# Kernel tuning notes

Measured on AMD Instinct MI355X. Metric: run time of the kernel, lower is better.

Reference implementation:

```python
import jax, jax.numpy as jnp
import numpy as np

B, S, D, H, ATT = 2048, 200, 64, 64, 64  # batch, hist_len, embed_dim, hidden, attention_size


def _xavier(k, shape):
    fan_out, fan_in = shape
    std = (2.0 / (fan_in + fan_out)) ** 0.5
    return (jax.random.normal(k, shape, jnp.float32) * std).astype(jnp.float32)


def setup_inputs() -> dict:
    key = jax.random.key(0)
    ks = jax.random.split(key, 12)
    return {
        "behavior": jax.random.normal(ks[0], (B, S, D), jnp.float32),
        "target": jax.random.normal(ks[1], (B, D), jnp.float32),
        "lengths": jax.random.randint(ks[2], (B,), 1, S + 1),
        # Interest-extraction GRU (torch nn.GRU layout: gates [r|z|n])
        "Wih": _xavier(ks[3], (3 * H, D)),
        "Whh": _xavier(ks[4], (3 * H, H)),
        "bih": jnp.zeros((3 * H,), jnp.float32),
        "bhh": jnp.zeros((3 * H,), jnp.float32),
        # Evolution attention MLP: Linear(H+D -> ATT) + ReLU + Linear(ATT -> 1, no bias)
        "A1": _xavier(ks[5], (ATT, H + D)),
        "b1": jnp.zeros((ATT,), jnp.float32),
        "A2": _xavier(ks[6], (1, ATT)),
        # Attentional GRU gates: Linear(input+hidden -> hidden)
        "Wr": _xavier(ks[7], (H, 2 * H)),
        "br": jnp.zeros((H,), jnp.float32),
        "Wz": _xavier(ks[8], (H, 2 * H)),
        "bz": jnp.zeros((H,), jnp.float32),
        "Wn": _xavier(ks[9], (H, 2 * H)),
        "bn": jnp.zeros((H,), jnp.float32),
    }


def _forward(behavior, target, lengths, Wih, Whh, bih, bhh, A1, b1, A2, Wr, br, Wz, bz, Wn, bn):
    Bsz, Slen, Din = behavior.shape
    Hs = Whh.shape[1]
    dt = behavior.dtype
    # (B, S) validity mask for padded positions (pack_padded_sequence semantics)
    mask = jnp.arange(Slen)[None, :] < lengths[:, None]

    # ---- Interest Extraction: masked GRU over time (lax.scan) ----
    gi_all = jnp.einsum('bsd,gd->sbg', behavior, Wih) + bih  # (S, B, 3H), input gates precomputed
    valid_t = jnp.moveaxis(mask, 0, 1)[..., None]            # (S, B, 1)

    def gru_step(h, inp):
        gi, v = inp
        gh = h @ Whh.T + bhh
        ir, iz, inn = jnp.split(gi, 3, axis=-1)
        hr, hz, hn = jnp.split(gh, 3, axis=-1)
        r = jax.nn.sigmoid(ir + hr)
        z = jax.nn.sigmoid(iz + hz)
        n = jnp.tanh(inn + r * hn)
        hnew = (1.0 - z) * n + z * h
        hnew = jnp.where(v, hnew, h)          # hold state past sequence end
        out = jnp.where(v, hnew, jnp.zeros_like(hnew))  # padded outputs are zero
        return hnew, out

    h0 = jnp.zeros((Bsz, Hs), dt)
    _, outs = jax.lax.scan(gru_step, h0, (gi_all, valid_t))  # outs: (S, B, H)
    hidden_states = jnp.moveaxis(outs, 0, 1)                 # (B, S, H)

    # ---- Interest Evolution: concat-MLP attention + masked softmax ----
    tgt = jnp.broadcast_to(target[:, None, :], (Bsz, Slen, Din))
    comb = jnp.concatenate([hidden_states, tgt], axis=-1)    # (B, S, H+D)
    att = jax.nn.relu(comb @ A1.T + b1) @ A2.T               # (B, S, 1)
    scores = jnp.where(mask, att[..., 0], jnp.asarray(-1e9, dt))
    att_w = jax.nn.softmax(scores, axis=1)[..., None]        # (B, S, 1)

    # ---- Attentional GRU scan over timesteps ----
    w_t = jnp.moveaxis(att_w, 0, 1)                          # (S, B, 1)

    def agru_step(h, inp):
        hi, ai = inp                                         # (B,H), (B,1)
        cat = jnp.concatenate([hi, h], axis=-1)
        r = jax.nn.sigmoid(cat @ Wr.T + br)
        z = jax.nn.sigmoid(cat @ Wz.T + bz) * ai             # attention-gated update gate
        catr = jnp.concatenate([hi, r * h], axis=-1)
        n = jnp.tanh(catr @ Wn.T + bn)
        return (1.0 - z) * h + z * n, None

    h_final, _ = jax.lax.scan(agru_step, jnp.zeros((Bsz, Hs), dt), (outs, w_t))
    return h_final  # (B, H)


def reference(behavior, target, lengths, Wih, Whh, bih, bhh, A1, b1, A2, Wr, br, Wz, bz, Wn, bn):
    return _forward(behavior, target, lengths, Wih, Whh, bih, bhh, A1, b1, A2, Wr, br, Wz, bz, Wn, bn)
```

## Files before the change

### kernel.cpp

```cpp
#include <hip/hip_runtime.h>

#define SLEN 200
#define NB   2048
#define CS   40

typedef short  bf8s   __attribute__((ext_vector_type(8)));
typedef __bf16 bf16x8 __attribute__((ext_vector_type(8)));
typedef float  f4     __attribute__((ext_vector_type(4)));

__device__ __forceinline__ short fb1(float x){ __bf16 b=(__bf16)x; return __builtin_bit_cast(short,b); }
__device__ __forceinline__ float b2f(unsigned short b){
  return __builtin_bit_cast(float, ((unsigned int)b)<<16);
}
__device__ __forceinline__ float ldf(const void* p, long i, bool bf){
  return bf ? b2f(((const unsigned short*)p)[i]) : ((const float*)p)[i];
}
__device__ __forceinline__ bf8s loadfrag(const void* p, long i, bool bf){
  bf8s r;
  if (bf) {
    r = *(const bf8s*)((const unsigned short*)p + i);
  } else {
    const float* q = (const float*)p + i;
#pragma unroll
    for (int k=0;k<8;k++) r[k] = fb1(q[k]);
  }
  return r;
}
__device__ __forceinline__ float rcp_(float x){ return __builtin_amdgcn_rcpf(x); }
__device__ __forceinline__ float sigm(float x){ return rcp_(1.f + __expf(-x)); }
__device__ __forceinline__ float tanh_(float x){ return 1.f - 2.f*rcp_(1.f + __expf(2.f*x)); }
__device__ __forceinline__ f4 MF(bf8s a, bf8s b, f4 c){
  return __builtin_amdgcn_mfma_f32_16x16x32_bf16(
    __builtin_bit_cast(bf16x8,a), __builtin_bit_cast(bf16x8,b), c, 0,0,0);
}
__device__ __forceinline__ void sync_lds(){
  asm volatile("s_waitcnt lgkmcnt(0)" ::: "memory");
  __builtin_amdgcn_s_barrier();
  __builtin_amdgcn_sched_barrier(0);
}

__global__ __launch_bounds__(256)
void k0_prep(const unsigned int* wds, int nw, const int* lengths, int* flag, int* perm){
  __shared__ int hist[256];
  __shared__ int base[256];
  __shared__ int cnt[256];
  __shared__ int wsum[4];
  const int tid = threadIdx.x;
  int c = 0;
  for (int i=tid;i<nw;i+=256){
    unsigned e = (wds[i] >> 7) & 0xFFu;
    c += (e >= 96u && e <= 160u) ? 1 : 0;
  }
  cnt[tid]=c; hist[tid]=0;
  __syncthreads();
  for (int s=128;s>0;s>>=1){
    if (tid<s) cnt[tid]+=cnt[tid+s];
    __syncthreads();
  }
  if (tid==0) flag[0] = (cnt[0]*2 > nw) ? 1 : 0;
  for (int i=tid;i<NB;i+=256) atomicAdd(&hist[lengths[i]&255],1);
  __syncthreads();
  {
    const int lane=tid&63, w=tid>>6;
    int v = hist[tid];
    int sum = v;
#pragma unroll
    for (int d=1; d<64; d<<=1){
      int o = __shfl_up(sum, d);
      if (lane >= d) sum += o;
    }
    if (lane==63) wsum[w]=sum;
    __syncthreads();
    int woff=0;
#pragma unroll
    for (int k=0;k<4;++k) if (k<w) woff+=wsum[k];
    base[tid] = woff + sum - v;
  }
  __syncthreads();
  for (int i=tid;i<NB;i+=256){
    int l=lengths[i]&255;
    int p=atomicAdd(&base[l],1);
    perm[p]=i;
  }
}

__global__ __launch_bounds__(256,1)
void fused(const void* behavior, const void* target, const int* lengths,
           const void* Wih, const void* Whh, const void* bih, const void* bhh,
           const void* A1, const void* b1, const void* A2,
           const void* Wr, const void* br, const void* Wz, const void* bz,
           const void* Wn, const void* bn,
           const int* perm, const int* flag,
           unsigned short* hidden, float* out){
  const bool bf = flag[0]!=0;
  const int tid=threadIdx.x, lane=tid&63, w=tid>>6, l15=lane&15, q=lane>>4;
  const int g0 = blockIdx.x*8;
  const int xrow = ((l15>>2)<<1)|(l15&1);

  __shared__ alignas(16) unsigned short x_s[2][CS][8][72];
  __shared__ alignas(16) unsigned short h_lds[2][16][72];
  __shared__ alignas(16) unsigned short h_hist[16][8][72];
  __shared__ alignas(16) unsigned short rh_lds[16][72];
  __shared__ float att_l[8][200];
  __shared__ float score_s[8][208];
  __shared__ float ct_s[8][64];
  __shared__ alignas(16) unsigned short tg_s[8][72];
  __shared__ float a2_s[64];
  __shared__ int rows8[8], lens8[8];

  if (tid<8){ int r=perm[g0+tid]; rows8[tid]=r; lens8[tid]=lengths[r]; }
  for (int i=tid;i<2*16*72;i+=256) ((unsigned short*)h_lds)[i]=0;
  for (int i=tid;i<16*72;i+=256)   ((unsigned short*)rh_lds)[i]=0;
  __syncthreads();

  int maxlen=1;
#pragma unroll
  for (int i=0;i<8;++i) maxlen = max(maxlen, lens8[i]);
  const int ml1 = maxlen-1;
  const int jc = w*16 + l15;

  const unsigned short* bp=(const unsigned short*)behavior;
  const float*          fp=(const float*)behavior;

  uint4 xr[10];
  auto issue_g = [&](const unsigned short* src, int t0){
#pragma unroll
    for (int it=0; it<10; ++it){
      int i=it*256+tid, row=i/320, k=i-row*320;
      int t=min(t0+(k>>3), ml1), d0=(k&7)*8;
      xr[it] = *(const uint4*)(src + (long)rows8[row]*(SLEN*64) + t*64 + d0);
    }
  };
  auto write_s = [&](int b_){
#pragma unroll
    for (int it=0; it<10; ++it){
      int i=it*256+tid, row=i/320, k=i-row*320;
      *(uint4*)&x_s[b_][k>>3][row][(k&7)*8] = xr[it];
    }
  };
  auto f32_stage = [&](int b_, int t0){
#pragma unroll
    for (int it=0; it<10; ++it){
      int i=it*256+tid, row=i/320, k=i-row*320;
      int t=min(t0+(k>>3), ml1), d0=(k&7)*8;
      const float* s = fp + (long)rows8[row]*(SLEN*64) + t*64 + d0;
      f4 a=*(const f4*)s, b2=*(const f4*)(s+4);
      bf8s v;
#pragma unroll
      for (int j=0;j<4;++j){ v[j]=fb1(a[j]); v[4+j]=fb1(b2[j]); }
      *(bf8s*)&x_s[b_][k>>3][row][d0] = v;
    }
  };
  auto dump_window = [&](int tbase){
    int dt = tid>>5, row=(tid>>2)&7, cs=(tid&3)*16;
    int t = tbase+dt;
    if (t < lens8[row]){
      uint4 v0 = *(const uint4*)&h_hist[t&15][row][cs];
      uint4 v1 = *(const uint4*)&h_hist[t&15][row][cs+8];
      long o = ((long)rows8[row]*SLEN + t)*64 + cs;
      *(uint4*)&hidden[o]   = v0;
      *(uint4*)&hidden[o+8] = v1;
    }
  };

  {
    bf8s wif[3][2], whf[3][2];
#pragma unroll
    for (int G=0;G<3;++G)
#pragma unroll
      for (int kf=0;kf<2;++kf){
        long off = (long)(G*64+jc)*64 + kf*32 + q*8;
        wif[G][kf] = loadfrag(Wih, off, bf);
        whf[G][kf] = loadfrag(Whh, off, bf);
      }
    const float Br  = ldf(bih,jc,bf)+ldf(bhh,jc,bf);
    const float Bz  = ldf(bih,64+jc,bf)+ldf(bhh,64+jc,bf);
    const float Bin = ldf(bih,128+jc,bf);
    const float Bhn = ldf(bhh,128+jc,bf);
    int Ln2[2];
#pragma unroll
    for (int i=0;i<2;++i) Ln2[i] = lens8[2*q+i];
    float hreg[2]={0.f,0.f};

    if (bf){ issue_g(bp,0); write_s(0); if (maxlen>CS) issue_g(bp,CS); }
    else   { f32_stage(0,0); }
    __syncthreads();

    int c=0;
    for (int t0=0; t0<maxlen; t0+=CS, ++c){
      const int tend = min(t0+CS, maxlen);
      for (int t=t0; t<tend; ++t){
        if ((t&7)==0 && t>=8) dump_window(t-8);
        const int tc = t-t0;
        bf8s xa0 = *(const bf8s*)&x_s[c&1][tc][xrow][q*8];
        bf8s xa1 = *(const bf8s*)&x_s[c&1][tc][xrow][32+q*8];
        bf8s ha0 = *(const bf8s*)&h_lds[t&1][l15][q*8];
        bf8s ha1 = *(const bf8s*)&h_lds[t&1][l15][32+q*8];

        f4 Tr  = {Br,Br,Br,Br};
        f4 Tz  = {Bz,Bz,Bz,Bz};
        f4 Txn = {Bin,Bin,Bin,Bin};
        f4 Thn = {Bhn,Bhn,Bhn,Bhn};
        Tr =MF(xa0,wif[0][0],Tr );  Tr =MF(xa1,wif[0][1],Tr );
        Tz =MF(xa0,wif[1][0],Tz );  Tz =MF(xa1,wif[1][1],Tz );
        Txn=MF(xa0,wif[2][0],Txn);  Txn=MF(xa1,wif[2][1],Txn);
        Tr =MF(ha0,whf[0][0],Tr );  Tr =MF(ha1,whf[0][1],Tr );
        Tz =MF(ha0,whf[1][0],Tz );  Tz =MF(ha1,whf[1][1],Tz );
        Thn=MF(ha0,whf[2][0],Thn); Thn=MF(ha1,whf[2][1],Thn);

        const int nb_=(t+1)&1;
#pragma unroll
        for (int i=0;i<2;++i){
          const int ar = 4*q+i;
          const int b_ = 2*q+i;
          float rg = sigm(Tr[i]);
          float zg = sigm(Tz[i]);
          float ng = tanh_(Txn[i] + rg*Thn[i]);
          float hold = hreg[i];
          float hnew = (1.f-zg)*ng + zg*hold;
          float hv = (t < Ln2[i]) ? hnew : hold;
          hreg[i] = hv;
          unsigned short hb16 = (unsigned short)fb1(hv);
          h_lds[nb_][ar][jc] = hb16;
          h_hist[t&15][b_][jc] = hb16;
        }
        sync_lds();
      }
      if (t0+CS < maxlen){
        if (bf){ write_s((c+1)&1); if (t0+2*CS < maxlen) issue_g(bp, t0+2*CS); }
        else   { f32_stage((c+1)&1, t0+CS); }
        sync_lds();
      }
    }
    dump_window((maxlen-1)&~7);
    asm volatile("s_waitcnt vmcnt(0)" ::: "memory");
  }
  __syncthreads();

  for (int i=tid;i<8*64;i+=256){
    int r=i>>6, c2=i&63;
    tg_s[r][c2] = (unsigned short)fb1(ldf(target,(long)rows8[r]*64 + c2, bf));
  }
  if (tid<64) a2_s[tid]=ldf(A2,tid,bf);
  __syncthreads();

  {
    {
      bf8s a1c0 = loadfrag(A1,(long)(w*16+l15)*128 + 64 + q*8, bf);
      bf8s a1c1 = loadfrag(A1,(long)(w*16+l15)*128 + 96 + q*8, bf);
      bf8s tgf0 = *(const bf8s*)&tg_s[l15&7][q*8];
      bf8s tgf1 = *(const bf8s*)&tg_s[l15&7][32+q*8];
      f4 Dct={0.f,0.f,0.f,0.f};
      Dct=MF(a1c0,tgf0,Dct);
      Dct=MF(a1c1,tgf1,Dct);
      if (l15<8){
#pragma unroll
        for (int i=0;i<4;++i)
          ct_s[l15][w*16+4*q+i] = Dct[i] + ldf(b1,w*16+4*q+i,bf);
      }
    }
    bf8s a1f[4][2];
#pragma unroll
    for (int nt=0;nt<4;++nt)
#pragma unroll
      for (int kf=0;kf<2;++kf)
        a1f[nt][kf] = loadfrag(A1,(long)(nt*16+l15)*128 + kf*32 + q*8, bf);
    __syncthreads();

#pragma unroll
    for (int rr=0;rr<2;++rr){
      int r = 2*w+rr, lenr = lens8[r];
      int mtr = (lenr+15)>>4; if (mtr>13) mtr=13;
      for (int mt=0; mt<mtr; ++mt){
        const unsigned short* hp = &hidden[((long)rows8[r]*SLEN + mt*16+l15)*64 + q*8];
        bf8s h0 = *(const bf8s*)hp;
        bf8s h1 = *(const bf8s*)(hp+32);
        f4 acc[4];
#pragma unroll
        for (int nt=0;nt<4;++nt){
          f4 a={0.f,0.f,0.f,0.f};
          a=MF(h0,a1f[nt][0],a); a=MF(h1,a1f[nt][1],a); acc[nt]=a;
        }
#pragma unroll
        for (int i=0;i<4;++i){
          float s=0.f;
#pragma unroll
          for (int nt=0;nt<4;++nt){
            int au = nt*16 + l15;
            s += fmaxf(acc[nt][i]+ct_s[r][au],0.f)*a2_s[au];
          }
#pragma unroll
          for (int d=1; d<16; d<<=1) s += __shfl_xor(s,d);
          if (l15==0) score_s[r][mt*16+4*q+i] = s;
        }
      }
      int t0=lane, t1=64+lane, t2=128+lane, t3=192+lane;
      float v0=(t0<lenr)?score_s[r][t0]:-3e38f;
      float v1=(t1<lenr)?score_s[r][t1]:-3e38f;
      float v2=(t2<lenr)?score_s[r][t2]:-3e38f;
      float v3=(t3<lenr)?score_s[r][t3]:-3e38f;
      float m = fmaxf(fmaxf(v0,v1),fmaxf(v2,v3));
#pragma unroll
      for (int d=32;d>0;d>>=1) m = fmaxf(m,__shfl_xor(m,d));
      float e0=(t0<lenr)?__expf(v0-m):0.f;
      float e1=(t1<lenr)?__expf(v1-m):0.f;
      float e2=(t2<lenr)?__expf(v2-m):0.f;
      float e3=(t3<lenr)?__expf(v3-m):0.f;
      float S = e0+e1+e2+e3;
#pragma unroll
      for (int d=32;d>0;d>>=1) S += __shfl_xor(S,d);
      float Si = rcp_(S);
      att_l[r][t0] = e0*Si;
      att_l[r][t1] = e1*Si;
      if (t2<200) att_l[r][t2] = e2*Si;
      if (t3<200) att_l[r][t3] = e3*Si;
    }
  }
  __syncthreads();

  for (int i=tid;i<2*16*72;i+=256) ((unsigned short*)h_lds)[i]=0;

  bf8s wrf[2][2], wzf[2][2], wnf[2][2];
#pragma unroll
  for (int hh=0;hh<2;++hh)
#pragma unroll
    for (int kf=0;kf<2;++kf){
      long off = (long)jc*128 + hh*64 + kf*32 + q*8;
      wrf[hh][kf]=loadfrag(Wr,off,bf);
      wzf[hh][kf]=loadfrag(Wz,off,bf);
      wnf[hh][kf]=loadfrag(Wn,off,bf);
    }
  const float Brv=ldf(br,jc,bf), Bzv=ldf(bz,jc,bf), Bnv=ldf(bn,jc,bf);

  float h3[2]={0.f,0.f};
  const long hbase = (long)rows8[xrow]*(SLEN*64) + q*8;
  bf8s hb00,hb01,hb10,hb11;
  {
    long o1 = hbase + (long)min(1,ml1)*64;
    hb00=*(const bf8s*)(hidden+hbase); hb01=*(const bf8s*)(hidden+hbase+32);
    hb10=*(const bf8s*)(hidden+o1);    hb11=*(const bf8s*)(hidden+o1+32);
  }
  __syncthreads();

  for (int t=0;t<maxlen;++t){
    long po = hbase + (long)min(t+2,ml1)*64;
    bf8s pN0 = *(const bf8s*)(hidden+po);
    bf8s pN1 = *(const bf8s*)(hidden+po+32);

    bf8s ha0=*(const bf8s*)&h_lds[t&1][l15][q*8];
    bf8s ha1=*(const bf8s*)&h_lds[t&1][l15][32+q*8];

    f4 Tr = {Brv,Brv,Brv,Brv};
    f4 Tz = {Bzv,Bzv,Bzv,Bzv};
    f4 Tn = {Bnv,Bnv,Bnv,Bnv};
    Tr=MF(hb00,wrf[0][0],Tr); Tr=MF(hb01,wrf[0][1],Tr);
    Tz=MF(hb00,wzf[0][0],Tz); Tz=MF(hb01,wzf[0][1],Tz);
    Tn=MF(hb00,wnf[0][0],Tn); Tn=MF(hb01,wnf[0][1],Tn);
    Tr=MF(ha0, wrf[1][0],Tr); Tr=MF(ha1, wrf[1][1],Tr);
    Tz=MF(ha0, wzf[1][0],Tz); Tz=MF(ha1, wzf[1][1],Tz);

    float zs[2], hs[2];
#pragma unroll
    for (int i=0;i<2;++i){
      const int ar = 4*q+i;
      const int b_ = 2*q+i;
      float rg = sigm(Tr[i]);
      float ai = att_l[b_][t];
      float zg = sigm(Tz[i]) * ai;
      float hold = h3[i];
      zs[i]=zg; hs[i]=hold;
      rh_lds[ar][jc] = (unsigned short)fb1(rg*hold);
    }
    sync_lds();

    bf8s ra0 = *(const bf8s*)&rh_lds[l15][q*8];
    bf8s ra1 = *(const bf8s*)&rh_lds[l15][32+q*8];
    Tn=MF(ra0,wnf[1][0],Tn); Tn=MF(ra1,wnf[1][1],Tn);

    const int nb_=(t+1)&1;
#pragma unroll
    for (int i=0;i<2;++i){
      const int ar = 4*q+i;
      float ng = tanh_(Tn[i]);
      float hnew = (zs[i]==0.f) ? hs[i] : hs[i] + zs[i]*(ng - hs[i]);
      h3[i] = hnew;
      h_lds[nb_][ar][jc] = (unsigned short)fb1(hnew);
    }
    hb00=hb10; hb01=hb11; hb10=pN0; hb11=pN1;
    sync_lds();
  }
#pragma unroll
  for (int i=0;i<2;++i)
    out[(long)rows8[2*q+i]*64 + jc] = h3[i];
}

extern "C" void kernel_launch(void* const* d_in, const int* in_sizes, int n_in,
                              void* d_out, int out_size, void* d_ws, size_t ws_size,
                              hipStream_t stream) {
  const void* behavior = d_in[0];
  const void* target   = d_in[1];
  const int*  lengths  = (const int*)d_in[2];
  const void* Wih = d_in[3];
  const void* Whh = d_in[4];
  const void* bih = d_in[5];
  const void* bhh = d_in[6];
  const void* A1  = d_in[7];
  const void* b1  = d_in[8];
  const void* A2  = d_in[9];
  const void* Wr  = d_in[10];
  const void* br  = d_in[11];
  const void* Wz  = d_in[12];
  const void* bz  = d_in[13];
  const void* Wn  = d_in[14];
  const void* bn  = d_in[15];

  int* flag = (int*)d_ws;
  unsigned short* hidden = (unsigned short*)((char*)d_ws + 256);
  int* perm = (int*)((char*)d_ws + 256 + (size_t)NB*SLEN*64*2);
  size_t needed = 256 + (size_t)NB*SLEN*64*2 + (size_t)NB*4;
  if (ws_size < needed) return;

  k0_prep<<<1, 256, 0, stream>>>((const unsigned int*)behavior, 4096, lengths, flag, perm);
  fused<<<NB/8, 256, 0, stream>>>(behavior, target, lengths,
                                  Wih, Whh, bih, bhh, A1, b1, A2,
                                  Wr, br, Wz, bz, Wn, bn,
                                  perm, flag, hidden, (float*)d_out);
}
```

Baseline: 226.4 us.

## Split each block to four sequences, raise occupancy, prefetch x from global directly

Each block now handles 4 batch rows instead of 8, and the grid becomes 512 blocks. Launch bounds are raised to allow 3 blocks per CU, and the chunked LDS staging of behavior is removed. Input rows are instead prefetched two steps ahead straight into registers. The aim is more concurrent recurrent chains per CU, to hide the serial per-timestep latency, and a smaller LDS footprint. In exchange, MFMA tiles are only a quarter used (one useful row per 16-row group), and per-step global loads sit on the recurrence path.

New measurement: 347.9 us. +53.7%, slower.

```diff
diff --git a/kernel.cpp b/kernel.cpp
--- a/kernel.cpp
+++ b/kernel.cpp
@@ -2,7 +2,6 @@
 
 #define SLEN 200
 #define NB   2048
-#define CS   40
 
 typedef short  bf8s   __attribute__((ext_vector_type(8)));
 typedef __bf16 bf16x8 __attribute__((ext_vector_type(8)));
@@ -84,7 +83,7 @@
   }
 }
 
-__global__ __launch_bounds__(256,1)
+__global__ __launch_bounds__(256,3)
 void fused(const void* behavior, const void* target, const int* lengths,
            const void* Wih, const void* Whh, const void* bih, const void* bhh,
            const void* A1, const void* b1, const void* A2,
@@ -94,72 +93,40 @@
            unsigned short* hidden, float* out){
   const bool bf = flag[0]!=0;
   const int tid=threadIdx.x, lane=tid&63, w=tid>>6, l15=lane&15, q=lane>>4;
-  const int g0 = blockIdx.x*8;
-  const int xrow = ((l15>>2)<<1)|(l15&1);
-
-  __shared__ alignas(16) unsigned short x_s[2][CS][8][72];
+  const int g0 = (blockIdx.x & 255)*8 + (blockIdx.x >> 8)*4;
+  const int xb = l15>>2;
+
   __shared__ alignas(16) unsigned short h_lds[2][16][72];
-  __shared__ alignas(16) unsigned short h_hist[16][8][72];
+  __shared__ alignas(16) unsigned short h_hist[16][4][72];
   __shared__ alignas(16) unsigned short rh_lds[16][72];
-  __shared__ float att_l[8][200];
-  __shared__ float score_s[8][208];
-  __shared__ float ct_s[8][64];
-  __shared__ alignas(16) unsigned short tg_s[8][72];
+  __shared__ float att_l[4][200];
+  __shared__ float score_s[4][208];
+  __shared__ float ct_s[4][64];
+  __shared__ alignas(16) unsigned short tg_s[4][72];
   __shared__ float a2_s[64];
-  __shared__ int rows8[8], lens8[8];
-
-  if (tid<8){ int r=perm[g0+tid]; rows8[tid]=r; lens8[tid]=lengths[r]; }
+  __shared__ int rows4[4], lens4[4];
+
+  if (tid<4){ int r=perm[g0+tid]; rows4[tid]=r; lens4[tid]=lengths[r]; }
   for (int i=tid;i<2*16*72;i+=256) ((unsigned short*)h_lds)[i]=0;
   for (int i=tid;i<16*72;i+=256)   ((unsigned short*)rh_lds)[i]=0;
   __syncthreads();
 
   int maxlen=1;
 #pragma unroll
-  for (int i=0;i<8;++i) maxlen = max(maxlen, lens8[i]);
+  for (int i=0;i<4;++i) maxlen = max(maxlen, lens4[i]);
   const int ml1 = maxlen-1;
   const int jc = w*16 + l15;
 
   const unsigned short* bp=(const unsigned short*)behavior;
   const float*          fp=(const float*)behavior;
 
-  uint4 xr[10];
-  auto issue_g = [&](const unsigned short* src, int t0){
-#pragma unroll
-    for (int it=0; it<10; ++it){
-      int i=it*256+tid, row=i/320, k=i-row*320;
-      int t=min(t0+(k>>3), ml1), d0=(k&7)*8;
-      xr[it] = *(const uint4*)(src + (long)rows8[row]*(SLEN*64) + t*64 + d0);
-    }
-  };
-  auto write_s = [&](int b_){
-#pragma unroll
-    for (int it=0; it<10; ++it){
-      int i=it*256+tid, row=i/320, k=i-row*320;
-      *(uint4*)&x_s[b_][k>>3][row][(k&7)*8] = xr[it];
-    }
-  };
-  auto f32_stage = [&](int b_, int t0){
-#pragma unroll
-    for (int it=0; it<10; ++it){
-      int i=it*256+tid, row=i/320, k=i-row*320;
-      int t=min(t0+(k>>3), ml1), d0=(k&7)*8;
-      const float* s = fp + (long)rows8[row]*(SLEN*64) + t*64 + d0;
-      f4 a=*(const f4*)s, b2=*(const f4*)(s+4);
-      bf8s v;
-#pragma unroll
-      for (int j=0;j<4;++j){ v[j]=fb1(a[j]); v[4+j]=fb1(b2[j]); }
-      *(bf8s*)&x_s[b_][k>>3][row][d0] = v;
-    }
-  };
   auto dump_window = [&](int tbase){
-    int dt = tid>>5, row=(tid>>2)&7, cs=(tid&3)*16;
+    int dt = tid>>5, row=(tid>>3)&3, cs=(tid&7)*8;
     int t = tbase+dt;
-    if (t < lens8[row]){
+    if (t < lens4[row]){
       uint4 v0 = *(const uint4*)&h_hist[t&15][row][cs];
-      uint4 v1 = *(const uint4*)&h_hist[t&15][row][cs+8];
-      long o = ((long)rows8[row]*SLEN + t)*64 + cs;
-      *(uint4*)&hidden[o]   = v0;
-      *(uint4*)&hidden[o+8] = v1;
+      long o = ((long)rows4[row]*SLEN + t)*64 + cs;
+      *(uint4*)&hidden[o] = v0;
     }
   };
 
@@ -177,69 +144,77 @@
     const float Bz  = ldf(bih,64+jc,bf)+ldf(bhh,64+jc,bf);
     const float Bin = ldf(bih,128+jc,bf);
     const float Bhn = ldf(bhh,128+jc,bf);
-    int Ln2[2];
-#pragma unroll
-    for (int i=0;i<2;++i) Ln2[i] = lens8[2*q+i];
-    float hreg[2]={0.f,0.f};
-
-    if (bf){ issue_g(bp,0); write_s(0); if (maxlen>CS) issue_g(bp,CS); }
-    else   { f32_stage(0,0); }
-    __syncthreads();
-
-    int c=0;
-    for (int t0=0; t0<maxlen; t0+=CS, ++c){
-      const int tend = min(t0+CS, maxlen);
-      for (int t=t0; t<tend; ++t){
-        if ((t&7)==0 && t>=8) dump_window(t-8);
-        const int tc = t-t0;
-        bf8s xa0 = *(const bf8s*)&x_s[c&1][tc][xrow][q*8];
-        bf8s xa1 = *(const bf8s*)&x_s[c&1][tc][xrow][32+q*8];
-        bf8s ha0 = *(const bf8s*)&h_lds[t&1][l15][q*8];
-        bf8s ha1 = *(const bf8s*)&h_lds[t&1][l15][32+q*8];
-
-        f4 Tr  = {Br,Br,Br,Br};
-        f4 Tz  = {Bz,Bz,Bz,Bz};
-        f4 Txn = {Bin,Bin,Bin,Bin};
-        f4 Thn = {Bhn,Bhn,Bhn,Bhn};
-        Tr =MF(xa0,wif[0][0],Tr );  Tr =MF(xa1,wif[0][1],Tr );
-        Tz =MF(xa0,wif[1][0],Tz );  Tz =MF(xa1,wif[1][1],Tz );
-        Txn=MF(xa0,wif[2][0],Txn);  Txn=MF(xa1,wif[2][1],Txn);
-        Tr =MF(ha0,whf[0][0],Tr );  Tr =MF(ha1,whf[0][1],Tr );
-        Tz =MF(ha0,whf[1][0],Tz );  Tz =MF(ha1,whf[1][1],Tz );
-        Thn=MF(ha0,whf[2][0],Thn); Thn=MF(ha1,whf[2][1],Thn);
-
-        const int nb_=(t+1)&1;
-#pragma unroll
-        for (int i=0;i<2;++i){
-          const int ar = 4*q+i;
-          const int b_ = 2*q+i;
-          float rg = sigm(Tr[i]);
-          float zg = sigm(Tz[i]);
-          float ng = tanh_(Txn[i] + rg*Thn[i]);
-          float hold = hreg[i];
-          float hnew = (1.f-zg)*ng + zg*hold;
-          float hv = (t < Ln2[i]) ? hnew : hold;
-          hreg[i] = hv;
-          unsigned short hb16 = (unsigned short)fb1(hv);
-          h_lds[nb_][ar][jc] = hb16;
-          h_hist[t&15][b_][jc] = hb16;
+    const int LnQ = lens4[q];
+    float hreg = 0.f;
+
+    const long xbase = (long)rows4[xb]*(SLEN*64) + q*8;
+    bf8s xC0,xC1,xN0,xN1;
+    f4 c0,c1,c2,c3, n0,n1,n2,n3;
+    {
+      long o0=xbase, o1=xbase+(long)min(1,ml1)*64;
+      if (bf){
+        xC0=*(const bf8s*)(bp+o0); xC1=*(const bf8s*)(bp+o0+32);
+        xN0=*(const bf8s*)(bp+o1); xN1=*(const bf8s*)(bp+o1+32);
+      } else {
+        c0=*(const f4*)(fp+o0); c1=*(const f4*)(fp+o0+4); c2=*(const f4*)(fp+o0+32); c3=*(const f4*)(fp+o0+36);
+        n0=*(const f4*)(fp+o1); n1=*(const f4*)(fp+o1+4); n2=*(const f4*)(fp+o1+32); n3=*(const f4*)(fp+o1+36);
+      }
+    }
+
+    for (int t=0;t<maxlen;++t){
+      if ((t&7)==0 && t>=8) dump_window(t-8);
+      long po = xbase + (long)min(t+2,ml1)*64;
+      bf8s pN0,pN1; f4 p0,p1,p2,p3;
+      if (bf){ pN0=*(const bf8s*)(bp+po); pN1=*(const bf8s*)(bp+po+32); }
+      else   { p0=*(const f4*)(fp+po); p1=*(const f4*)(fp+po+4); p2=*(const f4*)(fp+po+32); p3=*(const f4*)(fp+po+36); }
+
+      bf8s ha0 = *(const bf8s*)&h_lds[t&1][l15][q*8];
+      bf8s ha1 = *(const bf8s*)&h_lds[t&1][l15][32+q*8];
+      bf8s xa0, xa1;
+      if (bf){ xa0=xC0; xa1=xC1; }
+      else {
+#pragma unroll
+        for (int j=0;j<4;++j){
+          xa0[j]=fb1(c0[j]); xa0[4+j]=fb1(c1[j]);
+          xa1[j]=fb1(c2[j]); xa1[4+j]=fb1(c3[j]);
         }
-        sync_lds();
-      }
-      if (t0+CS < maxlen){
-        if (bf){ write_s((c+1)&1); if (t0+2*CS < maxlen) issue_g(bp, t0+2*CS); }
-        else   { f32_stage((c+1)&1, t0+CS); }
-        sync_lds();
-      }
+      }
+
+      f4 Tr  = {Br,Br,Br,Br};
+      f4 Tz  = {Bz,Bz,Bz,Bz};
+      f4 Txn = {Bin,Bin,Bin,Bin};
+      f4 Thn = {Bhn,Bhn,Bhn,Bhn};
+      Tr =MF(xa0,wif[0][0],Tr );  Tr =MF(xa1,wif[0][1],Tr );
+      Tz =MF(xa0,wif[1][0],Tz );  Tz =MF(xa1,wif[1][1],Tz );
+      Txn=MF(xa0,wif[2][0],Txn);  Txn=MF(xa1,wif[2][1],Txn);
+      Tr =MF(ha0,whf[0][0],Tr );  Tr =MF(ha1,whf[0][1],Tr );
+      Tz =MF(ha0,whf[1][0],Tz );  Tz =MF(ha1,whf[1][1],Tz );
+      Thn=MF(ha0,whf[2][0],Thn);  Thn=MF(ha1,whf[2][1],Thn);
+
+      const int nb_=(t+1)&1;
+      {
+        float rg = sigm(Tr[0]);
+        float zg = sigm(Tz[0]);
+        float ng = tanh_(Txn[0] + rg*Thn[0]);
+        float hnew = (1.f-zg)*ng + zg*hreg;
+        float hv = (t < LnQ) ? hnew : hreg;
+        hreg = hv;
+        unsigned short hb16 = (unsigned short)fb1(hv);
+        h_lds[nb_][4*q][jc] = hb16;
+        h_hist[t&15][q][jc] = hb16;
+      }
+      if (bf){ xC0=xN0; xC1=xN1; xN0=pN0; xN1=pN1; }
+      else   { c0=n0;c1=n1;c2=n2;c3=n3; n0=p0;n1=p1;n2=p2;n3=p3; }
+      sync_lds();
     }
     dump_window((maxlen-1)&~7);
     asm volatile("s_waitcnt vmcnt(0)" ::: "memory");
   }
   __syncthreads();
 
-  for (int i=tid;i<8*64;i+=256){
+  for (int i=tid;i<4*64;i+=256){
     int r=i>>6, c2=i&63;
-    tg_s[r][c2] = (unsigned short)fb1(ldf(target,(long)rows8[r]*64 + c2, bf));
+    tg_s[r][c2] = (unsigned short)fb1(ldf(target,(long)rows4[r]*64 + c2, bf));
   }
   if (tid<64) a2_s[tid]=ldf(A2,tid,bf);
   __syncthreads();
@@ -248,12 +223,12 @@
     {
       bf8s a1c0 = loadfrag(A1,(long)(w*16+l15)*128 + 64 + q*8, bf);
       bf8s a1c1 = loadfrag(A1,(long)(w*16+l15)*128 + 96 + q*8, bf);
-      bf8s tgf0 = *(const bf8s*)&tg_s[l15&7][q*8];
-      bf8s tgf1 = *(const bf8s*)&tg_s[l15&7][32+q*8];
+      bf8s tgf0 = *(const bf8s*)&tg_s[l15&3][q*8];
+      bf8s tgf1 = *(const bf8s*)&tg_s[l15&3][32+q*8];
       f4 Dct={0.f,0.f,0.f,0.f};
       Dct=MF(a1c0,tgf0,Dct);
       Dct=MF(a1c1,tgf1,Dct);
-      if (l15<8){
+      if (l15<4){
 #pragma unroll
         for (int i=0;i<4;++i)
           ct_s[l15][w*16+4*q+i] = Dct[i] + ldf(b1,w*16+4*q+i,bf);
@@ -267,54 +242,51 @@
         a1f[nt][kf] = loadfrag(A1,(long)(nt*16+l15)*128 + kf*32 + q*8, bf);
     __syncthreads();
 
-#pragma unroll
-    for (int rr=0;rr<2;++rr){
-      int r = 2*w+rr, lenr = lens8[r];
-      int mtr = (lenr+15)>>4; if (mtr>13) mtr=13;
-      for (int mt=0; mt<mtr; ++mt){
-        const unsigned short* hp = &hidden[((long)rows8[r]*SLEN + mt*16+l15)*64 + q*8];
-        bf8s h0 = *(const bf8s*)hp;
-        bf8s h1 = *(const bf8s*)(hp+32);
-        f4 acc[4];
+    const int r = w, lenr = lens4[r];
+    int mtr = (lenr+15)>>4; if (mtr>13) mtr=13;
+    for (int mt=0; mt<mtr; ++mt){
+      const unsigned short* hp = &hidden[((long)rows4[r]*SLEN + mt*16+l15)*64 + q*8];
+      bf8s h0 = *(const bf8s*)hp;
+      bf8s h1 = *(const bf8s*)(hp+32);
+      f4 acc[4];
+#pragma unroll
+      for (int nt=0;nt<4;++nt){
+        f4 a={0.f,0.f,0.f,0.f};
+        a=MF(h0,a1f[nt][0],a); a=MF(h1,a1f[nt][1],a); acc[nt]=a;
+      }
+#pragma unroll
+      for (int i=0;i<4;++i){
+        float s=0.f;
 #pragma unroll
         for (int nt=0;nt<4;++nt){
-          f4 a={0.f,0.f,0.f,0.f};
-          a=MF(h0,a1f[nt][0],a); a=MF(h1,a1f[nt][1],a); acc[nt]=a;
+          int au = nt*16 + l15;
+          s += fmaxf(acc[nt][i]+ct_s[r][au],0.f)*a2_s[au];
         }
 #pragma unroll
-        for (int i=0;i<4;++i){
-          float s=0.f;
-#pragma unroll
-          for (int nt=0;nt<4;++nt){
-            int au = nt*16 + l15;
-            s += fmaxf(acc[nt][i]+ct_s[r][au],0.f)*a2_s[au];
-          }
-#pragma unroll
-          for (int d=1; d<16; d<<=1) s += __shfl_xor(s,d);
-          if (l15==0) score_s[r][mt*16+4*q+i] = s;
-        }
-      }
-      int t0=lane, t1=64+lane, t2=128+lane, t3=192+lane;
-      float v0=(t0<lenr)?score_s[r][t0]:-3e38f;
-      float v1=(t1<lenr)?score_s[r][t1]:-3e38f;
-      float v2=(t2<lenr)?score_s[r][t2]:-3e38f;
-      float v3=(t3<lenr)?score_s[r][t3]:-3e38f;
-      float m = fmaxf(fmaxf(v0,v1),fmaxf(v2,v3));
-#pragma unroll
-      for (int d=32;d>0;d>>=1) m = fmaxf(m,__shfl_xor(m,d));
-      float e0=(t0<lenr)?__expf(v0-m):0.f;
-      float e1=(t1<lenr)?__expf(v1-m):0.f;
-      float e2=(t2<lenr)?__expf(v2-m):0.f;
-      float e3=(t3<lenr)?__expf(v3-m):0.f;
-      float S = e0+e1+e2+e3;
-#pragma unroll
-      for (int d=32;d>0;d>>=1) S += __shfl_xor(S,d);
-      float Si = rcp_(S);
-      att_l[r][t0] = e0*Si;
-      att_l[r][t1] = e1*Si;
-      if (t2<200) att_l[r][t2] = e2*Si;
-      if (t3<200) att_l[r][t3] = e3*Si;
-    }
+        for (int d=1; d<16; d<<=1) s += __shfl_xor(s,d);
+        if (l15==0) score_s[r][mt*16+4*q+i] = s;
+      }
+    }
+    int t0=lane, t1=64+lane, t2=128+lane, t3=192+lane;
+    float v0=(t0<lenr)?score_s[r][t0]:-3e38f;
+    float v1=(t1<lenr)?score_s[r][t1]:-3e38f;
+    float v2=(t2<lenr)?score_s[r][t2]:-3e38f;
+    float v3=(t3<lenr)?score_s[r][t3]:-3e38f;
+    float m = fmaxf(fmaxf(v0,v1),fmaxf(v2,v3));
+#pragma unroll
+    for (int d=32;d>0;d>>=1) m = fmaxf(m,__shfl_xor(m,d));
+    float e0=(t0<lenr)?__expf(v0-m):0.f;
+    float e1=(t1<lenr)?__expf(v1-m):0.f;
+    float e2=(t2<lenr)?__expf(v2-m):0.f;
+    float e3=(t3<lenr)?__expf(v3-m):0.f;
+    float S = e0+e1+e2+e3;
+#pragma unroll
+    for (int d=32;d>0;d>>=1) S += __shfl_xor(S,d);
+    float Si = rcp_(S);
+    att_l[r][t0] = e0*Si;
+    att_l[r][t1] = e1*Si;
+    if (t2<200) att_l[r][t2] = e2*Si;
+    if (t3<200) att_l[r][t3] = e3*Si;
   }
   __syncthreads();
 
@@ -332,8 +304,8 @@
     }
   const float Brv=ldf(br,jc,bf), Bzv=ldf(bz,jc,bf), Bnv=ldf(bn,jc,bf);
 
-  float h3[2]={0.f,0.f};
-  const long hbase = (long)rows8[xrow]*(SLEN*64) + q*8;
+  float h3 = 0.f;
+  const long hbase = (long)rows4[xb]*(SLEN*64) + q*8;
   bf8s hb00,hb01,hb10,hb11;
   {
     long o1 = hbase + (long)min(1,ml1)*64;
@@ -359,17 +331,13 @@
     Tr=MF(ha0, wrf[1][0],Tr); Tr=MF(ha1, wrf[1][1],Tr);
     Tz=MF(ha0, wzf[1][0],Tz); Tz=MF(ha1, wzf[1][1],Tz);
 
-    float zs[2], hs[2];
-#pragma unroll
-    for (int i=0;i<2;++i){
-      const int ar = 4*q+i;
-      const int b_ = 2*q+i;
-      float rg = sigm(Tr[i]);
-      float ai = att_l[b_][t];
-      float zg = sigm(Tz[i]) * ai;
-      float hold = h3[i];
-      zs[i]=zg; hs[i]=hold;
-      rh_lds[ar][jc] = (unsigned short)fb1(rg*hold);
+    float zs, hs;
+    {
+      float rg = sigm(Tr[0]);
+      float ai = att_l[q][t];
+      zs = sigm(Tz[0]) * ai;
+      hs = h3;
+      rh_lds[4*q][jc] = (unsigned short)fb1(rg*hs);
     }
     sync_lds();
 
@@ -378,20 +346,16 @@
     Tn=MF(ra0,wnf[1][0],Tn); Tn=MF(ra1,wnf[1][1],Tn);
 
     const int nb_=(t+1)&1;
-#pragma unroll
-    for (int i=0;i<2;++i){
-      const int ar = 4*q+i;
-      float ng = tanh_(Tn[i]);
-      float hnew = (zs[i]==0.f) ? hs[i] : hs[i] + zs[i]*(ng - hs[i]);
-      h3[i] = hnew;
-      h_lds[nb_][ar][jc] = (unsigned short)fb1(hnew);
+    {
+      float ng = tanh_(Tn[0]);
+      float hnew = (zs==0.f) ? hs : hs + zs*(ng - hs);
+      h3 = hnew;
+      h_lds[nb_][4*q][jc] = (unsigned short)fb1(hnew);
     }
     hb00=hb10; hb01=hb11; hb10=pN0; hb11=pN1;
     sync_lds();
   }
-#pragma unroll
-  for (int i=0;i<2;++i)
-    out[(long)rows8[2*q+i]*64 + jc] = h3[i];
+  out[(long)rows4[q]*64 + jc] = h3;
 }
 
 extern "C" void kernel_launch(void* const* d_in, const int* in_sizes, int n_in,
@@ -421,8 +385,8 @@
   if (ws_size < needed) return;
 
   k0_prep<<<1, 256, 0, stream>>>((const unsigned int*)behavior, 4096, lengths, flag, perm);
-  fused<<<NB/8, 256, 0, stream>>>(behavior, target, lengths,
-                                  Wih, Whh, bih, bhh, A1, b1, A2,
-                                  Wr, br, Wz, bz, Wn, bn,
-                                  perm, flag, hidden, (float*)d_out);
-}
+  fused<<<512, 256, 0, stream>>>(behavior, target, lengths,
+                                 Wih, Whh, bih, bhh, A1, b1, A2,
+                                 Wr, br, Wz, bz, Wn, bn,
+                                 perm, flag, hidden, (float*)d_out);
+}
```

## Compute AGRU reset gate in transposed MFMA layout to drop per-step LDS round trip

Applied to the files above, without the earlier changes.

In the attentional GRU loop, the reset gate is now computed with transposed MFMA fragments (weights as the A operand), using a permuted row mapping so each lane directly holds r values matching its h fragment elements. r*h is formed in registers and fed straight into the candidate MFMA, removing the rh_lds store, one barrier and the reload per timestep. This costs four times as many MFMAs for the r gate, plus extra sigmoids per lane and more weight registers, in exchange for a shorter serial critical path. The CS macro is also inlined as a literal with no behavioural change.

Measured after the change: 264.4 us. +16.8%, slower.

```diff
diff --git a/kernel.cpp b/kernel.cpp
--- a/kernel.cpp
+++ b/kernel.cpp
@@ -2,7 +2,6 @@
 
 #define SLEN 200
 #define NB   2048
-#define CS   40
 
 typedef short  bf8s   __attribute__((ext_vector_type(8)));
 typedef __bf16 bf16x8 __attribute__((ext_vector_type(8)));
@@ -97,7 +96,7 @@
   const int g0 = blockIdx.x*8;
   const int xrow = ((l15>>2)<<1)|(l15&1);
 
-  __shared__ alignas(16) unsigned short x_s[2][CS][8][72];
+  __shared__ alignas(16) unsigned short x_s[2][40][8][72];
   __shared__ alignas(16) unsigned short h_lds[2][16][72];
   __shared__ alignas(16) unsigned short h_hist[16][8][72];
   __shared__ alignas(16) unsigned short rh_lds[16][72];
@@ -182,13 +181,13 @@
     for (int i=0;i<2;++i) Ln2[i] = lens8[2*q+i];
     float hreg[2]={0.f,0.f};
 
-    if (bf){ issue_g(bp,0); write_s(0); if (maxlen>CS) issue_g(bp,CS); }
+    if (bf){ issue_g(bp,0); write_s(0); if (maxlen>40) issue_g(bp,40); }
     else   { f32_stage(0,0); }
     __syncthreads();
 
     int c=0;
-    for (int t0=0; t0<maxlen; t0+=CS, ++c){
-      const int tend = min(t0+CS, maxlen);
+    for (int t0=0; t0<maxlen; t0+=40, ++c){
+      const int tend = min(t0+40, maxlen);
       for (int t=t0; t<tend; ++t){
         if ((t&7)==0 && t>=8) dump_window(t-8);
         const int tc = t-t0;
@@ -226,9 +225,9 @@
         }
         sync_lds();
       }
-      if (t0+CS < maxlen){
-        if (bf){ write_s((c+1)&1); if (t0+2*CS < maxlen) issue_g(bp, t0+2*CS); }
-        else   { f32_stage((c+1)&1, t0+CS); }
+      if (t0+40 < maxlen){
+        if (bf){ write_s((c+1)&1); if (t0+80 < maxlen) issue_g(bp, t0+80); }
+        else   { f32_stage((c+1)&1, t0+40); }
         sync_lds();
       }
     }
@@ -320,17 +319,35 @@
 
   for (int i=tid;i<2*16*72;i+=256) ((unsigned short*)h_lds)[i]=0;
 
-  bf8s wrf[2][2], wzf[2][2], wnf[2][2];
+  bf8s wrp[4][4];
+  f4 brp[4];
+#pragma unroll
+  for (int tt=0;tt<4;++tt){
+    int prow_l = 32*(tt>>1) + 8*(l15>>2) + 4*(tt&1) + (l15&3);
+#pragma unroll
+    for (int kf=0;kf<4;++kf){
+      bf8s v;
+#pragma unroll
+      for (int j=0;j<8;++j)
+        v[j] = fb1(ldf(Wr, (long)prow_l*128 + kf*32 + 8*q + j, bf));
+      wrp[tt][kf]=v;
+    }
+#pragma unroll
+    for (int i=0;i<4;++i){
+      int pr = 32*(tt>>1) + 8*q + 4*(tt&1) + i;
+      brp[tt][i] = ldf(br, pr, bf);
+    }
+  }
+  bf8s wzf[2][2], wnf[2][2];
 #pragma unroll
   for (int hh=0;hh<2;++hh)
 #pragma unroll
     for (int kf=0;kf<2;++kf){
       long off = (long)jc*128 + hh*64 + kf*32 + q*8;
-      wrf[hh][kf]=loadfrag(Wr,off,bf);
       wzf[hh][kf]=loadfrag(Wz,off,bf);
       wnf[hh][kf]=loadfrag(Wn,off,bf);
     }
-  const float Brv=ldf(br,jc,bf), Bzv=ldf(bz,jc,bf), Bnv=ldf(bn,jc,bf);
+  const float Bzv=ldf(bz,jc,bf), Bnv=ldf(bn,jc,bf);
 
   float h3[2]={0.f,0.f};
   const long hbase = (long)rows8[xrow]*(SLEN*64) + q*8;
@@ -350,39 +367,47 @@
     bf8s ha0=*(const bf8s*)&h_lds[t&1][l15][q*8];
     bf8s ha1=*(const bf8s*)&h_lds[t&1][l15][32+q*8];
 
-    f4 Tr = {Brv,Brv,Brv,Brv};
+    f4 Dr0=brp[0], Dr1=brp[1], Dr2=brp[2], Dr3=brp[3];
+    Dr0=MF(wrp[0][0],hb00,Dr0); Dr0=MF(wrp[0][1],hb01,Dr0);
+    Dr0=MF(wrp[0][2],ha0,Dr0);  Dr0=MF(wrp[0][3],ha1,Dr0);
+    Dr1=MF(wrp[1][0],hb00,Dr1); Dr1=MF(wrp[1][1],hb01,Dr1);
+    Dr1=MF(wrp[1][2],ha0,Dr1);  Dr1=MF(wrp[1][3],ha1,Dr1);
+    Dr2=MF(wrp[2][0],hb00,Dr2); Dr2=MF(wrp[2][1],hb01,Dr2);
+    Dr2=MF(wrp[2][2],ha0,Dr2);  Dr2=MF(wrp[2][3],ha1,Dr2);
+    Dr3=MF(wrp[3][0],hb00,Dr3); Dr3=MF(wrp[3][1],hb01,Dr3);
+    Dr3=MF(wrp[3][2],ha0,Dr3);  Dr3=MF(wrp[3][3],ha1,Dr3);
+
     f4 Tz = {Bzv,Bzv,Bzv,Bzv};
+    Tz=MF(hb00,wzf[0][0],Tz); Tz=MF(hb01,wzf[0][1],Tz);
+    Tz=MF(ha0, wzf[1][0],Tz); Tz=MF(ha1, wzf[1][1],Tz);
+
+    float rgv0[4],rgv1[4],rgv2[4],rgv3[4];
+#pragma unroll
+    for (int i=0;i<4;++i){ rgv0[i]=sigm(Dr0[i]); rgv1[i]=sigm(Dr1[i]);
+                           rgv2[i]=sigm(Dr2[i]); rgv3[i]=sigm(Dr3[i]); }
+    bf8s rha0, rha1;
+#pragma unroll
+    for (int j=0;j<4;++j){
+      rha0[j]   = fb1(rgv0[j] * b2f((unsigned short)ha0[j]));
+      rha0[4+j] = fb1(rgv1[j] * b2f((unsigned short)ha0[4+j]));
+      rha1[j]   = fb1(rgv2[j] * b2f((unsigned short)ha1[j]));
+      rha1[4+j] = fb1(rgv3[j] * b2f((unsigned short)ha1[4+j]));
+    }
+
     f4 Tn = {Bnv,Bnv,Bnv,Bnv};
-    Tr=MF(hb00,wrf[0][0],Tr); Tr=MF(hb01,wrf[0][1],Tr);
-    Tz=MF(hb00,wzf[0][0],Tz); Tz=MF(hb01,wzf[0][1],Tz);
     Tn=MF(hb00,wnf[0][0],Tn); Tn=MF(hb01,wnf[0][1],Tn);
-    Tr=MF(ha0, wrf[1][0],Tr); Tr=MF(ha1, wrf[1][1],Tr);
-    Tz=MF(ha0, wzf[1][0],Tz); Tz=MF(ha1, wzf[1][1],Tz);
-
-    float zs[2], hs[2];
+    Tn=MF(rha0,wnf[1][0],Tn); Tn=MF(rha1,wnf[1][1],Tn);
+
+    const int nb_=(t+1)&1;
 #pragma unroll
     for (int i=0;i<2;++i){
       const int ar = 4*q+i;
       const int b_ = 2*q+i;
-      float rg = sigm(Tr[i]);
       float ai = att_l[b_][t];
       float zg = sigm(Tz[i]) * ai;
+      float ng = tanh_(Tn[i]);
       float hold = h3[i];
-      zs[i]=zg; hs[i]=hold;
-      rh_lds[ar][jc] = (unsigned short)fb1(rg*hold);
-    }
-    sync_lds();
-
-    bf8s ra0 = *(const bf8s*)&rh_lds[l15][q*8];
-    bf8s ra1 = *(const bf8s*)&rh_lds[l15][32+q*8];
-    Tn=MF(ra0,wnf[1][0],Tn); Tn=MF(ra1,wnf[1][1],Tn);
-
-    const int nb_=(t+1)&1;
-#pragma unroll
-    for (int i=0;i<2;++i){
-      const int ar = 4*q+i;
-      float ng = tanh_(Tn[i]);
-      float hnew = (zs[i]==0.f) ? hs[i] : hs[i] + zs[i]*(ng - hs[i]);
+      float hnew = (zg==0.f) ? hold : hold + zg*(ng - hold);
       h3[i] = hnew;
       h_lds[nb_][ar][jc] = (unsigned short)fb1(hnew);
     }
```
